# Kernel optimization log

Measured on AMD Instinct MI355X. Metric: run time of the kernel, lower is better.

## Reference

```python
import jax, jax.numpy as jnp
import numpy as np
from jax import lax

H = 64            # hidden size
NUM_LAYERS = 3
EMBED_LEN = 128
B, T = 256, 2048


def _lstm_layer(x, Wih, Whh, bih, bhh):
    """x: [B, T, in]; returns full hidden sequence [B, T, H].
    PyTorch gate order: i, f, g, o."""
    Bn = x.shape[0]
    b = bih + bhh  # [4H]
    # Precompute input contribution for all timesteps: [T, B, 4H]
    xg = jnp.einsum('bti,gi->tbg', x, Wih) + b
    h0 = jnp.zeros((Bn, H), x.dtype)
    c0 = jnp.zeros((Bn, H), x.dtype)

    def step(carry, xg_t):
        h, c = carry
        gates = xg_t + h @ Whh.T  # [B, 4H]
        i, f, g, o = jnp.split(gates, 4, axis=-1)
        i = jax.nn.sigmoid(i)
        f = jax.nn.sigmoid(f)
        g = jnp.tanh(g)
        o = jax.nn.sigmoid(o)
        c = f * c + i * g
        h = o * jnp.tanh(c)
        return (h, c), h

    (_, _), hs = lax.scan(step, (h0, c0), xg)  # hs: [T, B, H]
    return jnp.swapaxes(hs, 0, 1)              # [B, T, H]


def setup_inputs() -> dict:
    key = jax.random.key(0)
    ks = jax.random.split(key, 20)
    k = 1.0 / np.sqrt(H)  # PyTorch default init bound

    def u(kk, shape):
        return jax.random.uniform(kk, shape, jnp.float32, -k, k)

    inp = {"x": jax.random.normal(ks[0], (B, 1, T), jnp.float32)}
    in_sizes = [1, H, H]
    idx = 1
    for l in range(NUM_LAYERS):
        inp[f"Wih{l}"] = u(ks[idx], (4 * H, in_sizes[l])); idx += 1
        inp[f"Whh{l}"] = u(ks[idx], (4 * H, H)); idx += 1
        inp[f"bih{l}"] = u(ks[idx], (4 * H,)); idx += 1
        inp[f"bhh{l}"] = u(ks[idx], (4 * H,)); idx += 1
    inp["fcW"] = u(ks[idx], (EMBED_LEN, H)); idx += 1
    inp["fcb"] = u(ks[idx], (EMBED_LEN,))
    return inp


def reference(x, Wih0, Whh0, bih0, bhh0,
              Wih1, Whh1, bih1, bhh1,
              Wih2, Whh2, bih2, bhh2,
              fcW, fcb):
    # forward: transpose [B,1,T] -> [B,T,1]
    h = jnp.swapaxes(x, 1, 2)
    h = _lstm_layer(h, Wih0, Whh0, bih0, bhh0)
    h = _lstm_layer(h, Wih1, Whh1, bih1, bhh1)
    h = _lstm_layer(h, Wih2, Whh2, bih2, bhh2)
    last = h[:, -1, :]              # [B, H]
    return last @ fcW.T + fcb       # [B, EMBED_LEN]
```

## Files before the change

kernel.cpp:

```cpp
#include <hip/hip_runtime.h>

#define T_LEN 2048
#define HID 64
#define EMB 128
#define WD 8
#define NWIN (T_LEN / WD)
#define NPH (NWIN + 4)

typedef _Float16 half2_t __attribute__((ext_vector_type(2)));
typedef unsigned uint4v __attribute__((ext_vector_type(4)));

#if __has_builtin(__builtin_amdgcn_exp2f)
#define EXP2F(x) __builtin_amdgcn_exp2f(x)
#else
#define EXP2F(x) exp2f(x)
#endif
#if __has_builtin(__builtin_amdgcn_rcpf)
#define RCPF(x) __builtin_amdgcn_rcpf(x)
#else
#define RCPF(x) (1.0f / (x))
#endif

#define LOG2E 1.4426950408889634f

__device__ __forceinline__ float fdot2(unsigned a, unsigned b, float c) {
    return __builtin_amdgcn_fdot2(__builtin_bit_cast(half2_t, a),
                                  __builtin_bit_cast(half2_t, b), c, false);
}

__device__ __forceinline__ float dotrow(const uint4v* w, const uint4v* g, float init) {
    float a0 = init, a1 = 0.f, a2 = 0.f, a3 = 0.f;
    #pragma unroll
    for (int q = 0; q < 8; ++q) {
        a0 = fdot2(w[q][0], g[q][0], a0);
        a1 = fdot2(w[q][1], g[q][1], a1);
        a2 = fdot2(w[q][2], g[q][2], a2);
        a3 = fdot2(w[q][3], g[q][3], a3);
    }
    return (a0 + a1) + (a2 + a3);
}

__device__ __forceinline__ uint4v pack8(float4 a, float4 b, float s) {
    half2_t h0{(_Float16)(a.x * s), (_Float16)(a.y * s)};
    half2_t h1{(_Float16)(a.z * s), (_Float16)(a.w * s)};
    half2_t h2{(_Float16)(b.x * s), (_Float16)(b.y * s)};
    half2_t h3{(_Float16)(b.z * s), (_Float16)(b.w * s)};
    uint4v q;
    q[0] = __builtin_bit_cast(unsigned, h0);
    q[1] = __builtin_bit_cast(unsigned, h1);
    q[2] = __builtin_bit_cast(unsigned, h2);
    q[3] = __builtin_bit_cast(unsigned, h3);
    return q;
}

__device__ __forceinline__ void cvt8(const float* __restrict__ Wp, float s, uint4v* dst) {
    const float4* p = reinterpret_cast<const float4*>(Wp);
    #pragma unroll
    for (int k = 0; k < 8; ++k) dst[k] = pack8(p[2 * k], p[2 * k + 1], s);
}

__global__ __launch_bounds__(512)
__attribute__((amdgpu_waves_per_eu(2, 2)))
void lstm3_fused(
    const float* __restrict__ x,
    const float* __restrict__ Wih0, const float* __restrict__ Whh0,
    const float* __restrict__ bih0, const float* __restrict__ bhh0,
    const float* __restrict__ Wih1, const float* __restrict__ Whh1,
    const float* __restrict__ bih1, const float* __restrict__ bhh1,
    const float* __restrict__ Wih2, const float* __restrict__ Whh2,
    const float* __restrict__ bih2, const float* __restrict__ bhh2,
    const float* __restrict__ fcW,  const float* __restrict__ fcb,
    float* __restrict__ out)
{
    const int b   = blockIdx.x;
    const int tid = threadIdx.x;
    const int wv  = tid >> 6;
    const int L   = tid & 63;

    __shared__ __align__(16) _Float16 h0ring[16][HID];
    __shared__ __align__(16) _Float16 h1ring[16][HID];
    __shared__ __align__(16) _Float16 h2ring[2][HID];
    __shared__ float p1buf[2][WD][4][HID];
    __shared__ float p2buf[2][WD][4][HID];
    __shared__ __align__(16) float xs[T_LEN];

    {
        const float4* xg4 = reinterpret_cast<const float4*>(x + b * T_LEN);
        reinterpret_cast<float4*>(xs)[tid] = xg4[tid];
        reinterpret_cast<unsigned*>(h0ring)[tid] = 0u;
        reinterpret_cast<unsigned*>(h1ring)[tid] = 0u;
        if (tid < 64) reinterpret_cast<unsigned*>(h2ring)[tid] = 0u;
    }

    const float sI = -LOG2E, sF = -LOG2E, sG = -2.f * LOG2E, sO = -LOG2E;
    const float scl[4] = {sI, sF, sG, sO};

    uint4v w[4][8];
    float bias4[4] = {0.f, 0.f, 0.f, 0.f};
    float wx4[4]   = {0.f, 0.f, 0.f, 0.f};

    if (wv < 3) {
        const float* Wh = (wv == 0) ? Whh0 : (wv == 1) ? Whh1 : Whh2;
        const float* bi = (wv == 0) ? bih0 : (wv == 1) ? bih1 : bih2;
        const float* bh = (wv == 0) ? bhh0 : (wv == 1) ? bhh1 : bhh2;
        #pragma unroll
        for (int c = 0; c < 4; ++c) {
            cvt8(Wh + (c * 64 + L) * 64, scl[c], w[c]);
            bias4[c] = (bi[c * 64 + L] + bh[c * 64 + L]) * scl[c];
        }
        if (wv == 0) {
            #pragma unroll
            for (int c = 0; c < 4; ++c) wx4[c] = Wih0[c * 64 + L] * scl[c];
        }
    } else if (wv == 4) {
        cvt8(Wih1 + (  0 + L) * 64, sI, w[0]);
    } else if (wv == 5) {
        cvt8(Wih1 + ( 64 + L) * 64, sF, w[0]);
    } else if (wv == 6) {
        cvt8(Wih1 + (128 + L) * 64, sG, w[0]);
    } else if (wv == 3) {
        cvt8(Wih1 + (192 + L) * 64, sO, w[0]);
        cvt8(Wih2 + (  0 + L) * 64, sI, w[1]);
    } else {
        cvt8(Wih2 + ( 64 + L) * 64, sF, w[0]);
        cvt8(Wih2 + (128 + L) * 64, sG, w[1]);
        cvt8(Wih2 + (192 + L) * 64, sO, w[2]);
    }

    float cst = 0.f;
    __syncthreads();

    for (int ph = 0; ph < NPH; ++ph) {
        const int par = ph & 1;

        if (wv == 0) {
            if (ph < NWIN) {
                _Float16* cur = &h0ring[par * 8][0];
                const _Float16* prv = &h0ring[(par ^ 1) * 8][0];
                const int tb = ph * WD;
                #pragma unroll
                for (int j = 0; j < WD; ++j) {
                    const uint4v* hp = reinterpret_cast<const uint4v*>(
                        (j == 0) ? (prv + 7 * HID) : (cur + (j - 1) * HID));
                    uint4v g[8];
                    #pragma unroll
                    for (int k = 0; k < 8; ++k) g[k] = hp[k];
                    float xv = xs[tb + j];
                    float d0 = dotrow(w[0], g, fmaf(wx4[0], xv, bias4[0]));
                    float d1 = dotrow(w[1], g, fmaf(wx4[1], xv, bias4[1]));
                    float d2 = dotrow(w[2], g, fmaf(wx4[2], xv, bias4[2]));
                    float d3 = dotrow(w[3], g, fmaf(wx4[3], xv, bias4[3]));
                    float ai = RCPF(1.f + EXP2F(d0));
                    float af = RCPF(1.f + EXP2F(d1));
                    float ag = fmaf(2.f, RCPF(1.f + EXP2F(d2)), -1.f);
                    float ao = RCPF(1.f + EXP2F(d3));
                    cst = fmaf(af, cst, ai * ag);
                    float tc = fmaf(2.f, RCPF(1.f + EXP2F(-2.f * LOG2E * cst)), -1.f);
                    cur[j * HID + L] = (_Float16)(ao * tc);
                }
            }
        } else if (wv == 1) {
            if (ph >= 2 && ph < NWIN + 2) {
                _Float16* cur = &h1ring[par * 8][0];
                const _Float16* prv = &h1ring[(par ^ 1) * 8][0];
                const float (*pb)[4][HID] = p1buf[par];
                #pragma unroll
                for (int j = 0; j < WD; ++j) {
                    const uint4v* hp = reinterpret_cast<const uint4v*>(
                        (j == 0) ? (prv + 7 * HID) : (cur + (j - 1) * HID));
                    uint4v g[8];
                    #pragma unroll
                    for (int k = 0; k < 8; ++k) g[k] = hp[k];
                    float d0 = dotrow(w[0], g, bias4[0] + pb[j][0][L]);
                    float d1 = dotrow(w[1], g, bias4[1] + pb[j][1][L]);
                    float d2 = dotrow(w[2], g, bias4[2] + pb[j][2][L]);
                    float d3 = dotrow(w[3], g, bias4[3] + pb[j][3][L]);
                    float ai = RCPF(1.f + EXP2F(d0));
                    float af = RCPF(1.f + EXP2F(d1));
                    float ag = fmaf(2.f, RCPF(1.f + EXP2F(d2)), -1.f);
                    float ao = RCPF(1.f + EXP2F(d3));
                    cst = fmaf(af, cst, ai * ag);
                    float tc = fmaf(2.f, RCPF(1.f + EXP2F(-2.f * LOG2E * cst)), -1.f);
                    cur[j * HID + L] = (_Float16)(ao * tc);
                }
            }
        } else if (wv == 2) {
            if (ph >= 4) {
                const float (*pb)[4][HID] = p2buf[par];
                #pragma unroll
                for (int j = 0; j < WD; ++j) {
                    const uint4v* hp = reinterpret_cast<const uint4v*>(
                        &h2ring[(j & 1) ^ 1][0]);
                    uint4v g[8];
                    #pragma unroll
                    for (int k = 0; k < 8; ++k) g[k] = hp[k];
                    float d0 = dotrow(w[0], g, bias4[0] + pb[j][0][L]);
                    float d1 = dotrow(w[1], g, bias4[1] + pb[j][1][L]);
                    float d2 = dotrow(w[2], g, bias4[2] + pb[j][2][L]);
                    float d3 = dotrow(w[3], g, bias4[3] + pb[j][3][L]);
                    float ai = RCPF(1.f + EXP2F(d0));
                    float af = RCPF(1.f + EXP2F(d1));
                    float ag = fmaf(2.f, RCPF(1.f + EXP2F(d2)), -1.f);
                    float ao = RCPF(1.f + EXP2F(d3));
                    cst = fmaf(af, cst, ai * ag);
                    float tc = fmaf(2.f, RCPF(1.f + EXP2F(-2.f * LOG2E * cst)), -1.f);
                    h2ring[j & 1][L] = (_Float16)(ao * tc);
                }
            }
        } else {
            const bool p1act = (ph >= 1 && ph < NWIN + 1);
            const bool p2act = (ph >= 3 && ph < NWIN + 3);
            if (wv == 4 || wv == 5 || wv == 6) {
                if (p1act) {
                    const _Float16* hw = &h0ring[(par ^ 1) * 8][0];
                    float (*po)[4][HID] = p1buf[par ^ 1];
                    const int c0 = wv - 4;
                    #pragma unroll
                    for (int j = 0; j < WD; ++j) {
                        const uint4v* hp = reinterpret_cast<const uint4v*>(hw + j * HID);
                        uint4v g[8];
                        #pragma unroll
                        for (int k = 0; k < 8; ++k) g[k] = hp[k];
                        po[j][c0][L] = dotrow(w[0], g, 0.f);
                    }
                }
            } else if (wv == 3) {
                if (p1act) {
                    const _Float16* hw = &h0ring[(par ^ 1) * 8][0];
                    float (*po)[4][HID] = p1buf[par ^ 1];
                    #pragma unroll
                    for (int j = 0; j < WD; ++j) {
                        const uint4v* hp = reinterpret_cast<const uint4v*>(hw + j * HID);
                        uint4v g[8];
                        #pragma unroll
                        for (int k = 0; k < 8; ++k) g[k] = hp[k];
                        po[j][3][L] = dotrow(w[0], g, 0.f);
                    }
                }
                if (p2act) {
                    const _Float16* hw = &h1ring[(par ^ 1) * 8][0];
                    float (*po)[4][HID] = p2buf[par ^ 1];
                    #pragma unroll
                    for (int j = 0; j < WD; ++j) {
                        const uint4v* hp = reinterpret_cast<const uint4v*>(hw + j * HID);
                        uint4v g[8];
                        #pragma unroll
                        for (int k = 0; k < 8; ++k) g[k] = hp[k];
                        po[j][0][L] = dotrow(w[1], g, 0.f);
                    }
                }
            } else {
                if (p2act) {
                    const _Float16* hw = &h1ring[(par ^ 1) * 8][0];
                    float (*po)[4][HID] = p2buf[par ^ 1];
                    #pragma unroll
                    for (int j = 0; j < WD; ++j) {
                        const uint4v* hp = reinterpret_cast<const uint4v*>(hw + j * HID);
                        uint4v g[8];
                        #pragma unroll
                        for (int k = 0; k < 8; ++k) g[k] = hp[k];
                        po[j][1][L] = dotrow(w[0], g, 0.f);
                        po[j][2][L] = dotrow(w[1], g, 0.f);
                        po[j][3][L] = dotrow(w[2], g, 0.f);
                    }
                }
            }
        }

        __syncthreads();
    }

    if (tid < EMB) {
        float acc = fcb[tid];
        const _Float16* hf = &h2ring[1][0];
        const float4* W4 = reinterpret_cast<const float4*>(fcW + tid * HID);
        #pragma unroll
        for (int k = 0; k < 16; ++k) {
            float4 wv4 = W4[k];
            acc = fmaf(wv4.x, (float)hf[4 * k + 0], acc);
            acc = fmaf(wv4.y, (float)hf[4 * k + 1], acc);
            acc = fmaf(wv4.z, (float)hf[4 * k + 2], acc);
            acc = fmaf(wv4.w, (float)hf[4 * k + 3], acc);
        }
        out[b * EMB + tid] = acc;
    }
}

extern "C" void kernel_launch(void* const* d_in, const int* in_sizes, int n_in,
                              void* d_out, int out_size, void* d_ws, size_t ws_size,
                              hipStream_t stream) {
    const float* x    = (const float*)d_in[0];
    const float* Wih0 = (const float*)d_in[1];
    const float* Whh0 = (const float*)d_in[2];
    const float* bih0 = (const float*)d_in[3];
    const float* bhh0 = (const float*)d_in[4];
    const float* Wih1 = (const float*)d_in[5];
    const float* Whh1 = (const float*)d_in[6];
    const float* bih1 = (const float*)d_in[7];
    const float* bhh1 = (const float*)d_in[8];
    const float* Wih2 = (const float*)d_in[9];
    const float* Whh2 = (const float*)d_in[10];
    const float* bih2 = (const float*)d_in[11];
    const float* bhh2 = (const float*)d_in[12];
    const float* fcW  = (const float*)d_in[13];
    const float* fcb  = (const float*)d_in[14];
    float* out = (float*)d_out;

    lstm3_fused<<<dim3(256), dim3(512), 0, stream>>>(
        x, Wih0, Whh0, bih0, bhh0,
        Wih1, Whh1, bih1, bhh1,
        Wih2, Whh2, bih2, bhh2,
        fcW, fcb, out);
}
```

Before: 974.8 us.

## Compute windowed input projections with MFMA on two waves instead of five

The per-window input projections for layers 1 and 2 (Wih times eight hidden vectors) move from fdot2 dot products spread over five helper waves onto 16x16x32 f16 MFMA instructions. One wave now handles each layer, with weights pre-packed into MFMA A-fragment layout and the hidden window loaded as B fragments. The partial buffers get padded rows to reduce LDS bank conflicts on the vector stores. The block still launches eight waves, so waves 4-6 now do no work, and half the MFMA columns are wasted because the window holds only eight timesteps.

```diff
diff --git a/kernel.cpp b/kernel.cpp
--- a/kernel.cpp
+++ b/kernel.cpp
@@ -6,8 +6,12 @@
 #define WD 8
 #define NWIN (T_LEN / WD)
 #define NPH (NWIN + 4)
+#define PPAD (HID + 4)
 
 typedef _Float16 half2_t __attribute__((ext_vector_type(2)));
+typedef _Float16 half4 __attribute__((ext_vector_type(4)));
+typedef _Float16 half8 __attribute__((ext_vector_type(8)));
+typedef float f32x4 __attribute__((ext_vector_type(4)));
 typedef unsigned uint4v __attribute__((ext_vector_type(4)));
 
 #if __has_builtin(__builtin_amdgcn_exp2f)
@@ -80,8 +84,8 @@
     __shared__ __align__(16) _Float16 h0ring[16][HID];
     __shared__ __align__(16) _Float16 h1ring[16][HID];
     __shared__ __align__(16) _Float16 h2ring[2][HID];
-    __shared__ float p1buf[2][WD][4][HID];
-    __shared__ float p2buf[2][WD][4][HID];
+    __shared__ __align__(16) float p1buf[2][WD][4][PPAD];
+    __shared__ __align__(16) float p2buf[2][WD][4][PPAD];
     __shared__ __align__(16) float xs[T_LEN];
 
     {
@@ -112,19 +116,26 @@
             #pragma unroll
             for (int c = 0; c < 4; ++c) wx4[c] = Wih0[c * 64 + L] * scl[c];
         }
-    } else if (wv == 4) {
-        cvt8(Wih1 + (  0 + L) * 64, sI, w[0]);
-    } else if (wv == 5) {
-        cvt8(Wih1 + ( 64 + L) * 64, sF, w[0]);
-    } else if (wv == 6) {
-        cvt8(Wih1 + (128 + L) * 64, sG, w[0]);
-    } else if (wv == 3) {
-        cvt8(Wih1 + (192 + L) * 64, sO, w[0]);
-        cvt8(Wih2 + (  0 + L) * 64, sI, w[1]);
-    } else {
-        cvt8(Wih2 + ( 64 + L) * 64, sF, w[0]);
-        cvt8(Wih2 + (128 + L) * 64, sG, w[1]);
-        cvt8(Wih2 + (192 + L) * 64, sO, w[2]);
+    } else if (wv == 3 || wv == 7) {
+        const float* Wsrc = (wv == 3) ? Wih1 : Wih2;
+        const int g4 = (L >> 4) * 4;
+        const int mr = L & 15;
+        #pragma unroll
+        for (int t = 0; t < 16; ++t) {
+            const float s = scl[t >> 2];
+            const float* rowp = Wsrc + (t * 16 + mr) * 64;
+            #pragma unroll
+            for (int kf = 0; kf < 2; ++kf) {
+                float4 lo = *reinterpret_cast<const float4*>(rowp + kf * 32 + g4);
+                float4 hi = *reinterpret_cast<const float4*>(rowp + kf * 32 + 16 + g4);
+                half8 a = {(_Float16)(lo.x * s), (_Float16)(lo.y * s),
+                           (_Float16)(lo.z * s), (_Float16)(lo.w * s),
+                           (_Float16)(hi.x * s), (_Float16)(hi.y * s),
+                           (_Float16)(hi.z * s), (_Float16)(hi.w * s)};
+                const int idx = t * 2 + kf;
+                w[idx >> 3][idx & 7] = __builtin_bit_cast(uint4v, a);
+            }
+        }
     }
 
     float cst = 0.f;
@@ -163,7 +174,7 @@
             if (ph >= 2 && ph < NWIN + 2) {
                 _Float16* cur = &h1ring[par * 8][0];
                 const _Float16* prv = &h1ring[(par ^ 1) * 8][0];
-                const float (*pb)[4][HID] = p1buf[par];
+                const float (*pb)[4][PPAD] = p1buf[par];
                 #pragma unroll
                 for (int j = 0; j < WD; ++j) {
                     const uint4v* hp = reinterpret_cast<const uint4v*>(
@@ -186,7 +197,7 @@
             }
         } else if (wv == 2) {
             if (ph >= 4) {
-                const float (*pb)[4][HID] = p2buf[par];
+                const float (*pb)[4][PPAD] = p2buf[par];
                 #pragma unroll
                 for (int j = 0; j < WD; ++j) {
                     const uint4v* hp = reinterpret_cast<const uint4v*>(
@@ -207,61 +218,36 @@
                     h2ring[j & 1][L] = (_Float16)(ao * tc);
                 }
             }
-        } else {
-            const bool p1act = (ph >= 1 && ph < NWIN + 1);
-            const bool p2act = (ph >= 3 && ph < NWIN + 3);
-            if (wv == 4 || wv == 5 || wv == 6) {
-                if (p1act) {
-                    const _Float16* hw = &h0ring[(par ^ 1) * 8][0];
-                    float (*po)[4][HID] = p1buf[par ^ 1];
-                    const int c0 = wv - 4;
+        } else if (wv == 3 || wv == 7) {
+            const bool act = (wv == 3) ? (ph >= 1 && ph < NWIN + 1)
+                                       : (ph >= 3 && ph < NWIN + 3);
+            if (act) {
+                const _Float16 (*ring)[HID] = (wv == 3) ? h0ring : h1ring;
+                float (*po)[4][PPAD] = ((wv == 3) ? p1buf : p2buf)[par ^ 1];
+                const int jj = L & 7;
+                const int g4 = (L >> 4) * 4;
+                const _Float16* rb = &ring[(par ^ 1) * 8 + jj][0];
+                half4 b00 = *reinterpret_cast<const half4*>(rb + g4);
+                half4 b01 = *reinterpret_cast<const half4*>(rb + 16 + g4);
+                half4 b10 = *reinterpret_cast<const half4*>(rb + 32 + g4);
+                half4 b11 = *reinterpret_cast<const half4*>(rb + 48 + g4);
+                half8 B0 = __builtin_shufflevector(b00, b01, 0, 1, 2, 3, 4, 5, 6, 7);
+                half8 B1 = __builtin_shufflevector(b10, b11, 0, 1, 2, 3, 4, 5, 6, 7);
+                f32x4 acc[16];
+                #pragma unroll
+                for (int t = 0; t < 16; ++t) {
+                    const int i0 = t * 2, i1 = t * 2 + 1;
+                    f32x4 z = {0.f, 0.f, 0.f, 0.f};
+                    acc[t] = __builtin_amdgcn_mfma_f32_16x16x32_f16(
+                        __builtin_bit_cast(half8, w[i0 >> 3][i0 & 7]), B0, z, 0, 0, 0);
+                    acc[t] = __builtin_amdgcn_mfma_f32_16x16x32_f16(
+                        __builtin_bit_cast(half8, w[i1 >> 3][i1 & 7]), B1, acc[t], 0, 0, 0);
+                }
+                if ((L & 15) < 8) {
                     #pragma unroll
-                    for (int j = 0; j < WD; ++j) {
-                        const uint4v* hp = reinterpret_cast<const uint4v*>(hw + j * HID);
-                        uint4v g[8];
-                        #pragma unroll
-                        for (int k = 0; k < 8; ++k) g[k] = hp[k];
-                        po[j][c0][L] = dotrow(w[0], g, 0.f);
-                    }
-                }
-            } else if (wv == 3) {
-                if (p1act) {
-                    const _Float16* hw = &h0ring[(par ^ 1) * 8][0];
-                    float (*po)[4][HID] = p1buf[par ^ 1];
-                    #pragma unroll
-                    for (int j = 0; j < WD; ++j) {
-                        const uint4v* hp = reinterpret_cast<const uint4v*>(hw + j * HID);
-                        uint4v g[8];
-                        #pragma unroll
-                        for (int k = 0; k < 8; ++k) g[k] = hp[k];
-                        po[j][3][L] = dotrow(w[0], g, 0.f);
-                    }
-                }
-                if (p2act) {
-                    const _Float16* hw = &h1ring[(par ^ 1) * 8][0];
-                    float (*po)[4][HID] = p2buf[par ^ 1];
-                    #pragma unroll
-                    for (int j = 0; j < WD; ++j) {
-                        const uint4v* hp = reinterpret_cast<const uint4v*>(hw + j * HID);
-                        uint4v g[8];
-                        #pragma unroll
-                        for (int k = 0; k < 8; ++k) g[k] = hp[k];
-                        po[j][0][L] = dotrow(w[1], g, 0.f);
-                    }
-                }
-            } else {
-                if (p2act) {
-                    const _Float16* hw = &h1ring[(par ^ 1) * 8][0];
-                    float (*po)[4][HID] = p2buf[par ^ 1];
-                    #pragma unroll
-                    for (int j = 0; j < WD; ++j) {
-                        const uint4v* hp = reinterpret_cast<const uint4v*>(hw + j * HID);
-                        uint4v g[8];
-                        #pragma unroll
-                        for (int k = 0; k < 8; ++k) g[k] = hp[k];
-                        po[j][1][L] = dotrow(w[0], g, 0.f);
-                        po[j][2][L] = dotrow(w[1], g, 0.f);
-                        po[j][3][L] = dotrow(w[2], g, 0.f);
+                    for (int t = 0; t < 16; ++t) {
+                        *reinterpret_cast<f32x4*>(
+                            &po[jj][t >> 2][(t & 3) * 16 + g4]) = acc[t];
                     }
                 }
             }
```

Measured after the change: 1.021 ms. 4.8% more time.
